# Optimization experiments

Measured on AMD Instinct MI355X. Metric: run time of the kernel, lower is better.

## Reference

```python
import jax, jax.numpy as jnp
import numpy as np

B, C, N, DI, DC = 64, 32, 1152, 8, 16
ROUTINGS = 3


def squash(x, axis=-1):
    sq = jnp.sum(x * x, axis=axis, keepdims=True)
    scale = sq / (1.0 + sq) / jnp.sqrt(sq + 1e-07)
    return scale * x


def setup_inputs() -> dict:
    key = jax.random.key(0)
    k1, k2 = jax.random.split(key)
    inputs = jax.random.normal(k1, (B, N, DI), dtype=jnp.float32)
    # Xavier-uniform init for W[n_caps, n_in, d_cap, d_in]; fan computed over last two dims
    limit = float(np.sqrt(6.0 / (DC + DI)))
    W = jax.random.uniform(k2, (C, N, DC, DI), dtype=jnp.float32, minval=-limit, maxval=limit)
    return {"inputs": inputs, "W": W}


def reference(inputs, W):
    # inputs_hat[b,c,n,i] = sum_j W[c,n,i,j] * inputs[b,n,j]
    inputs_hat = jnp.einsum('cnij,bnj->bcni', W, inputs)  # [B,C,N,DC]
    b = jnp.zeros((B, C, N), dtype=inputs_hat.dtype)
    outputs = None
    for i in range(ROUTINGS):
        c = jax.nn.softmax(b, axis=1)                      # over output capsules
        s = jnp.einsum('bcn,bcni->bci', c, inputs_hat)     # weighted sum over input caps
        outputs = squash(s)                                # [B,C,DC]
        if i < ROUTINGS - 1:
            agreement = jnp.einsum('bci,bcni->bcn', outputs, inputs_hat)
            b = b + agreement
    return outputs
```

## Files before the change

### kernel.cpp

```cpp
#include <hip/hip_runtime.h>
#include <hip/hip_bf16.h>
#include <hip/hip_fp16.h>

#define B_  64
#define C_  32
#define N_  1152
#define DI_ 8
#define DC_ 16
#define STH 512

#define HCH 2
#define HSLOT 192
#define NOCT 24

#define FCH 3
#define FSLOT 128

static __device__ __forceinline__ unsigned pkh(float a, float b) {
    __half2 t = __float22half2_rn(make_float2(a, b));
    return *reinterpret_cast<unsigned*>(&t);
}
static __device__ __forceinline__ float2 uph(unsigned u) {
    __half2 h; *reinterpret_cast<unsigned*>(&h) = u;
    return __half22float2(h);
}

__global__ __launch_bounds__(STH, 2) void caps_hat(
    const float* __restrict__ X, const float* __restrict__ W,
    uint4* __restrict__ hatg, __half2* __restrict__ p1)
{
    __shared__ float wlds[HCH * 64 * 64];

    const int xcd  = blockIdx.x & 7;
    const int k    = blockIdx.x >> 3;
    const int bg   = k & 3;
    const int slot = 24 * xcd + (k >> 2);

    const int tid  = threadIdx.x;
    const int lane = tid & 63;
    const int c    = lane & 31;
    const int h    = lane >> 5;
    const int le   = 2 * c + h;
    const int sw   = c & 7;
    const int wu   = __builtin_amdgcn_readfirstlane(tid) >> 6;
    const int bl0  = wu * 2;

    const int g_nl[4] = { (tid) >> 10, (tid + 512) >> 10, (tid + 1024) >> 10, (tid + 1536) >> 10 };
    const int g_f [4] = { (tid >> 4) & 63, ((tid + 512) >> 4) & 63, ((tid + 1024) >> 4) & 63, ((tid + 1536) >> 4) & 63 };
    const int g_q  = tid & 15;

    float acc[2][8];
#pragma unroll
    for (int bq = 0; bq < 2; bq++)
#pragma unroll
        for (int r = 0; r < 8; r++) acc[bq][r] = 0.f;

    float4 wreg[4];
    {
        const int n0 = slot * HCH;
#pragma unroll
        for (int i = 0; i < 4; i++) {
            const int wc = g_f[i] >> 1, wh = g_f[i] & 1;
            wreg[i] = *(const float4*)(W + (size_t)(wc * N_ + n0 + g_nl[i]) * 128 + wh * 64 + g_q * 4);
        }
#pragma unroll
        for (int i = 0; i < 4; i++) {
            const int wc = g_f[i] >> 1;
            *(float4*)(wlds + (g_nl[i] * 64 + g_f[i]) * 64 + (g_q ^ (wc & 7)) * 4) = wreg[i];
        }
    }
    __syncthreads();

    for (int cc = 0; cc < 3; cc++) {
        if (cc < 2) {
            const int n0 = (slot + (cc + 1) * HSLOT) * HCH;
#pragma unroll
            for (int i = 0; i < 4; i++) {
                const int wc = g_f[i] >> 1, wh = g_f[i] & 1;
                wreg[i] = *(const float4*)(W + (size_t)(wc * N_ + n0 + g_nl[i]) * 128 + wh * 64 + g_q * 4);
            }
        }
        const int n0 = (slot + cc * HSLOT) * HCH;

#pragma unroll
        for (int nl = 0; nl < HCH; nl++) {
            float4 xa[2], xb[2];
#pragma unroll
            for (int bq = 0; bq < 2; bq++) {
                const float* xp = X + ((size_t)(bg * 16 + bl0 + bq) * N_ + n0 + nl) * DI_;
                xa[bq] = *(const float4*)xp;
                xb[bq] = *(const float4*)(xp + 4);
            }
            uint4 hq[2];
            const float* frag = wlds + (nl * 64 + le) * 64;
#pragma unroll
            for (int rp = 0; rp < 4; rp++) {
                const int r0 = 2 * rp, r1 = r0 + 1;
                const int pa0 = ((2 * r0) ^ sw) * 4;
                const int pb0 = pa0 ^ 4;
                const int pa1 = ((2 * r1) ^ sw) * 4;
                const int pb1 = pa1 ^ 4;
                const float4 wa0 = *(const float4*)(frag + pa0);
                const float4 wb0 = *(const float4*)(frag + pb0);
                const float4 wa1 = *(const float4*)(frag + pa1);
                const float4 wb1 = *(const float4*)(frag + pb1);
#pragma unroll
                for (int bq = 0; bq < 2; bq++) {
                    const float hv0 = wa0.x*xa[bq].x + wa0.y*xa[bq].y + wa0.z*xa[bq].z + wa0.w*xa[bq].w
                                    + wb0.x*xb[bq].x + wb0.y*xb[bq].y + wb0.z*xb[bq].z + wb0.w*xb[bq].w;
                    const float hv1 = wa1.x*xa[bq].x + wa1.y*xa[bq].y + wa1.z*xa[bq].z + wa1.w*xa[bq].w
                                    + wb1.x*xb[bq].x + wb1.y*xb[bq].y + wb1.z*xb[bq].z + wb1.w*xb[bq].w;
                    acc[bq][r0] += hv0;
                    acc[bq][r1] += hv1;
                    (&hq[bq].x)[rp] = pkh(hv0, hv1);
                }
            }
#pragma unroll
            for (int bq = 0; bq < 2; bq++) {
                const int b = bg * 16 + bl0 + bq;
                hatg[(size_t)(b * N_ + n0 + nl) * 64 + le] = hq[bq];
            }
        }

        __syncthreads();
        if (cc < 2) {
#pragma unroll
            for (int i = 0; i < 4; i++) {
                const int wc = g_f[i] >> 1;
                *(float4*)(wlds + (g_nl[i] * 64 + g_f[i]) * 64 + (g_q ^ (wc & 7)) * 4) = wreg[i];
            }
            __syncthreads();
        }
    }

    __half2* pout = p1 + (size_t)(bg * HSLOT + slot) * (16 * 256);
#pragma unroll
    for (int bq = 0; bq < 2; bq++) {
        uint4 st;
        st.x = pkh(acc[bq][0]*0.03125f, acc[bq][1]*0.03125f);
        st.y = pkh(acc[bq][2]*0.03125f, acc[bq][3]*0.03125f);
        st.z = pkh(acc[bq][4]*0.03125f, acc[bq][5]*0.03125f);
        st.w = pkh(acc[bq][6]*0.03125f, acc[bq][7]*0.03125f);
        *(uint4*)(pout + (bl0 + bq) * 256 + le * 4) = st;
    }
}

__global__ __launch_bounds__(STH, 2) void caps_route(
    const uint4* __restrict__ hatg, const float* __restrict__ accb,
    float* __restrict__ p2)
{
    __shared__ float red[8 * 512];
    const int xcd  = blockIdx.x & 7;
    const int rest = blockIdx.x >> 3;
    const int ug   = rest % 3;
    const int b    = rest / 3;
    const int u    = 8 * ug + xcd;
    const int tid  = threadIdx.x;
    const int w    = tid >> 6;
    const int lane = tid & 63;
    const int c    = lane & 31;
    const int h    = lane >> 5;
    const int le   = 2 * c + h;

    const float* ap = accb + (size_t)b * 512 + le * 8;
    const float4 a0 = *(const float4*)ap;
    const float4 a1 = *(const float4*)(ap + 4);

    const uint4* hb = hatg + (size_t)(b * N_ + u * 48) * 64 + le;

    uint4 v[6];
#pragma unroll
    for (int m = 0; m < 6; m++)
        v[m] = hb[(size_t)(w + 8 * m) * 64];

    float lg[6], sm[6];
#pragma unroll
    for (int m = 0; m < 6; m++) {
        const float2 f0 = uph(v[m].x);
        const float2 f1 = uph(v[m].y);
        const float2 f2 = uph(v[m].z);
        const float2 f3 = uph(v[m].w);
        lg[m] = f0.x*a0.x + f0.y*a0.y + f1.x*a0.z + f1.y*a0.w
              + f2.x*a1.x + f2.y*a1.y + f3.x*a1.z + f3.y*a1.w;
    }
#pragma unroll
    for (int m = 0; m < 6; m++) lg[m] += __shfl_xor(lg[m], 32, 64);
#pragma unroll
    for (int m = 0; m < 6; m++) { lg[m] = __expf(lg[m]); sm[m] = lg[m]; }
#pragma unroll
    for (int d = 16; d >= 1; d >>= 1)
#pragma unroll
        for (int m = 0; m < 6; m++) sm[m] += __shfl_xor(sm[m], d, 64);

    float acc[8] = {0.f,0.f,0.f,0.f,0.f,0.f,0.f,0.f};
#pragma unroll
    for (int m = 0; m < 6; m++) {
        const float sc = lg[m] * __builtin_amdgcn_rcpf(sm[m]);
        const float2 f0 = uph(v[m].x);
        const float2 f1 = uph(v[m].y);
        const float2 f2 = uph(v[m].z);
        const float2 f3 = uph(v[m].w);
        acc[0] += sc * f0.x; acc[1] += sc * f0.y;
        acc[2] += sc * f1.x; acc[3] += sc * f1.y;
        acc[4] += sc * f2.x; acc[5] += sc * f2.y;
        acc[6] += sc * f3.x; acc[7] += sc * f3.y;
    }
    *(float4*)(red + w * 512 + le * 8)     = make_float4(acc[0], acc[1], acc[2], acc[3]);
    *(float4*)(red + w * 512 + le * 8 + 4) = make_float4(acc[4], acc[5], acc[6], acc[7]);
    __syncthreads();
    float vs = 0.f;
#pragma unroll
    for (int s = 0; s < 8; s++) vs += red[s * 512 + tid];
    p2[(size_t)(b * NOCT + u) * 512 + tid] = vs;
}

__global__ __launch_bounds__(512) void caps_r1(
    const __half2* __restrict__ p1, float* __restrict__ accb,
    float* __restrict__ out, int t)
{
    const int b   = blockIdx.x >> 2;
    const int q   = blockIdx.x & 3;
    const int tid = threadIdx.x;
    const int ep  = tid >> 3;
    const int p   = tid & 7;
    const int bg  = b >> 4, bl = b & 15;
    const __half2* base = p1 + (size_t)bg * HSLOT * 4096 + bl * 256 + (q * 64 + ep);
    float vx = 0.f, vy = 0.f;
#pragma unroll 8
    for (int ch = p; ch < HSLOT; ch += 8) {
        const float2 f = __half22float2(base[(size_t)ch * 4096]);
        vx += f.x; vy += f.y;
    }
    vx += __shfl_xor(vx, 1, 64);  vy += __shfl_xor(vy, 1, 64);
    vx += __shfl_xor(vx, 2, 64);  vy += __shfl_xor(vy, 2, 64);
    vx += __shfl_xor(vx, 4, 64);  vy += __shfl_xor(vy, 4, 64);
    float sq = vx * vx + vy * vy;
    sq += __shfl_xor(sq, 8, 64);
    sq += __shfl_xor(sq, 16, 64);
    sq += __shfl_xor(sq, 32, 64);
    const float scale = sq / (1.f + sq) * rsqrtf(sq + 1e-7f);
    if (p == 0) {
        const int oidx = b * 512 + q * 128 + ep * 2;
        const float ox = vx * scale, oy = vy * scale;
        if (t == 2) { out[oidx] = ox; out[oidx + 1] = oy; }
        else if (t == 0) { accb[oidx] = ox; accb[oidx + 1] = oy; }
        else { accb[oidx] += ox; accb[oidx + 1] += oy; }
    }
}

__global__ __launch_bounds__(512) void caps_r2(
    const float* __restrict__ p2, float* __restrict__ accb,
    float* __restrict__ out, int t)
{
    const int b = blockIdx.x;
    const int e = threadIdx.x;
    const float* base = p2 + (size_t)b * (NOCT * 512) + e;
    float v = 0.f;
#pragma unroll
    for (int s = 0; s < NOCT; s++) v += base[s * 512];
    float sq = v * v;
#pragma unroll
    for (int m = 1; m <= 8; m <<= 1) sq += __shfl_xor(sq, m, 64);
    const float scale = sq / (1.f + sq) * rsqrtf(sq + 1e-7f);
    const float ov = v * scale;
    const int oidx = b * 512 + e;
    if (t == 2) out[oidx] = ov;
    else        accb[oidx] += ov;
}

__global__ __launch_bounds__(STH, 2) void caps_s_fb(
    const float* __restrict__ X, const float* __restrict__ W,
    const float* __restrict__ aout, float* __restrict__ partials, int t)
{
    __shared__ float wlds[FCH * 64 * 64];
    __shared__ float xlds[FCH * 16 * 8];
    const int bg = blockIdx.x & 3, slot = blockIdx.x >> 2;
    const int tid = threadIdx.x, w = tid >> 6, lane = tid & 63;
    const int c = lane & 31, h = lane >> 5, bl0 = w * 2, sw = c & 7;
    float areg[2][8] = {};
    if (t > 0) {
#pragma unroll
        for (int bq = 0; bq < 2; bq++) {
            const float* ap = aout + (size_t)(bg * 16 + bl0 + bq) * 512 + c * 16 + h * 8;
            const float4 a0 = *(const float4*)ap; const float4 a1 = *(const float4*)(ap + 4);
            areg[bq][0]=a0.x; areg[bq][1]=a0.y; areg[bq][2]=a0.z; areg[bq][3]=a0.w;
            areg[bq][4]=a1.x; areg[bq][5]=a1.y; areg[bq][6]=a1.z; areg[bq][7]=a1.w;
        }
    }
    float acc[2][8];
#pragma unroll
    for (int bq = 0; bq < 2; bq++)
#pragma unroll
        for (int r = 0; r < 8; r++) acc[bq][r] = 0.f;
    for (int cc = 0; cc < 3; cc++) {
        if (cc) __syncthreads();
        const int n0 = (slot + cc * FSLOT) * FCH;
        for (int G = tid; G < FCH * 1024; G += STH) {
            const int nl = G >> 10, f = (G >> 4) & 63, q = G & 15;
            const int wc = f >> 1, wh = f & 1;
            const float4 v = *(const float4*)(W + (size_t)(wc * N_ + n0 + nl) * 128 + wh * 64 + q * 4);
            *(float4*)(wlds + (nl * 64 + f) * 64 + (q ^ (wc & 7)) * 4) = v;
        }
        if (tid < FCH * 32) {
            const int nl = tid >> 5, bl = (tid >> 1) & 15, qx = tid & 1;
            const float4 v = *(const float4*)(X + (size_t)((bg * 16 + bl) * N_ + n0 + nl) * DI_ + qx * 4);
            *(float4*)(xlds + (nl * 16 + bl) * 8 + qx * 4) = v;
        }
        __syncthreads();
#pragma unroll
        for (int nl = 0; nl < FCH; nl++) {
            float4 xa[2], xb[2];
#pragma unroll
            for (int bq = 0; bq < 2; bq++) {
                const float* xp = xlds + (nl * 16 + bl0 + bq) * 8;
                xa[bq] = *(const float4*)xp; xb[bq] = *(const float4*)(xp + 4);
            }
            float hat[2][8];
            const float* frag = wlds + (nl * 64 + 2 * c + h) * 64;
#pragma unroll
            for (int r = 0; r < 8; r++) {
                const int pa = ((2 * r) ^ sw) * 4; const int pb = pa ^ 4;
                const float4 wa = *(const float4*)(frag + pa);
                const float4 wb = *(const float4*)(frag + pb);
#pragma unroll
                for (int bq = 0; bq < 2; bq++)
                    hat[bq][r] = wa.x*xa[bq].x + wa.y*xa[bq].y + wa.z*xa[bq].z + wa.w*xa[bq].w
                               + wb.x*xb[bq].x + wb.y*xb[bq].y + wb.z*xb[bq].z + wb.w*xb[bq].w;
            }
#pragma unroll
            for (int bq = 0; bq < 2; bq++) {
                float softc;
                if (t > 0) {
                    float lg = hat[bq][0]*areg[bq][0] + hat[bq][1]*areg[bq][1]
                             + hat[bq][2]*areg[bq][2] + hat[bq][3]*areg[bq][3]
                             + hat[bq][4]*areg[bq][4] + hat[bq][5]*areg[bq][5]
                             + hat[bq][6]*areg[bq][6] + hat[bq][7]*areg[bq][7];
                    lg += __shfl_xor(lg, 32, 64);
                    const float e = __expf(lg);
                    float s = e;
#pragma unroll
                    for (int m = 16; m >= 1; m >>= 1) s += __shfl_xor(s, m, 64);
                    softc = e / s;
                } else softc = 1.0f / 32.0f;
#pragma unroll
                for (int r = 0; r < 8; r++) acc[bq][r] += softc * hat[bq][r];
            }
        }
    }
    float* pout = partials + (size_t)(bg * FSLOT + slot) * (16 * 512);
#pragma unroll
    for (int bq = 0; bq < 2; bq++) {
        float* pb = pout + (bl0 + bq) * 512 + c * 16 + h * 8;
        *(float4*)pb       = make_float4(acc[bq][0], acc[bq][1], acc[bq][2], acc[bq][3]);
        *(float4*)(pb + 4) = make_float4(acc[bq][4], acc[bq][5], acc[bq][6], acc[bq][7]);
    }
}

__global__ __launch_bounds__(256) void caps_r1_fb(
    const float* __restrict__ partials, float* __restrict__ accb,
    float* __restrict__ out, int t)
{
    const int b   = blockIdx.x >> 2;
    const int q   = blockIdx.x & 3;
    const int tid = threadIdx.x;
    const int e   = q * 128 + (tid >> 1);
    const int p   = tid & 1;
    const int bg  = b >> 4, bl = b & 15;
    const float* base = partials + (size_t)bg * FSLOT * 8192 + (size_t)bl * 512 + e;
    float v = 0.f;
#pragma unroll 8
    for (int ch = p; ch < FSLOT; ch += 2)
        v += base[(size_t)ch * 8192];
    v += __shfl_xor(v, 1, 64);
    float sq = v * v;
#pragma unroll
    for (int m = 2; m <= 16; m <<= 1) sq += __shfl_xor(sq, m, 64);
    const float scale = sq / (1.f + sq) * rsqrtf(sq + 1e-7f);
    const float ov = v * scale;
    if (p == 0) {
        const int oidx = b * 512 + e;
        if (t == 2) out[oidx] = ov;
        else        accb[oidx] = (t == 0) ? ov : (accb[oidx] + ov);
    }
}

extern "C" void kernel_launch(void* const* d_in, const int* in_sizes, int n_in,
                              void* d_out, int out_size, void* d_ws, size_t ws_size,
                              hipStream_t stream) {
    const float* X = (const float*)d_in[0];
    const float* W = (const float*)d_in[1];
    float* out = (float*)d_out;

    const size_t hat_b = (size_t)B_ * N_ * 512 * 2;
    const size_t p1_b  = (size_t)4 * HSLOT * 4096 * 4;
    const size_t p2_b  = (size_t)B_ * NOCT * 512 * 4;
    const size_t acc_b = (size_t)B_ * 512 * 4;

    if (ws_size >= hat_b + p1_b + p2_b + acc_b) {
        char* ws = (char*)d_ws;
        uint4*   hatg = (uint4*)ws;
        __half2* p1   = (__half2*)(ws + hat_b);
        float*   p2   = (float*)(ws + hat_b + p1_b);
        float*   accb = (float*)(ws + hat_b + p1_b + p2_b);
        caps_hat  <<<768, STH, 0, stream>>>(X, W, hatg, p1);
        caps_r1   <<<256, 512, 0, stream>>>(p1, accb, out, 0);
        caps_route<<<B_ * NOCT, STH, 0, stream>>>(hatg, accb, p2);
        caps_r2   <<<64, 512, 0, stream>>>(p2, accb, out, 1);
        caps_route<<<B_ * NOCT, STH, 0, stream>>>(hatg, accb, p2);
        caps_r2   <<<64, 512, 0, stream>>>(p2, accb, out, 2);
    } else {
        float* partials = (float*)d_ws;
        float* accb = partials + (size_t)512 * 8192;
        for (int t = 0; t < 3; t++) {
            caps_s_fb<<<512, STH, 0, stream>>>(X, W, accb, partials, t);
            caps_r1_fb<<<256, 256, 0, stream>>>(partials, accb, out, t);
        }
    }
}
```

Baseline: 144.1 us.

## Halve batch per block in caps_hat, drop W register prefetch, split route softmax

caps_hat now gives each block 8 batch rows instead of 16, with one batch per wave, and launches twice as many blocks. The W register double-buffer is replaced by a plain load-to-LDS then sync each chunk. This cuts register pressure and raises parallelism, but every W tile is loaded from global memory twice as often and the W load is no longer overlapped with compute. caps_route's softmax is split into two groups of three to shorten live ranges, and the p1 layout and caps_r1 indexing are adjusted to match.

After: 129.7 us. -10.0%, faster.

```diff
diff --git a/kernel.cpp b/kernel.cpp
--- a/kernel.cpp
+++ b/kernel.cpp
@@ -33,8 +33,8 @@
 
     const int xcd  = blockIdx.x & 7;
     const int k    = blockIdx.x >> 3;
-    const int bg   = k & 3;
-    const int slot = 24 * xcd + (k >> 2);
+    const int bg   = k & 7;
+    const int slot = 24 * xcd + (k >> 3);
 
     const int tid  = threadIdx.x;
     const int lane = tid & 63;
@@ -43,55 +43,31 @@
     const int le   = 2 * c + h;
     const int sw   = c & 7;
     const int wu   = __builtin_amdgcn_readfirstlane(tid) >> 6;
-    const int bl0  = wu * 2;
-
-    const int g_nl[4] = { (tid) >> 10, (tid + 512) >> 10, (tid + 1024) >> 10, (tid + 1536) >> 10 };
-    const int g_f [4] = { (tid >> 4) & 63, ((tid + 512) >> 4) & 63, ((tid + 1024) >> 4) & 63, ((tid + 1536) >> 4) & 63 };
-    const int g_q  = tid & 15;
-
-    float acc[2][8];
-#pragma unroll
-    for (int bq = 0; bq < 2; bq++)
-#pragma unroll
-        for (int r = 0; r < 8; r++) acc[bq][r] = 0.f;
-
-    float4 wreg[4];
-    {
-        const int n0 = slot * HCH;
-#pragma unroll
-        for (int i = 0; i < 4; i++) {
-            const int wc = g_f[i] >> 1, wh = g_f[i] & 1;
-            wreg[i] = *(const float4*)(W + (size_t)(wc * N_ + n0 + g_nl[i]) * 128 + wh * 64 + g_q * 4);
-        }
-#pragma unroll
-        for (int i = 0; i < 4; i++) {
-            const int wc = g_f[i] >> 1;
-            *(float4*)(wlds + (g_nl[i] * 64 + g_f[i]) * 64 + (g_q ^ (wc & 7)) * 4) = wreg[i];
-        }
-    }
-    __syncthreads();
+    const int b    = bg * 8 + wu;
+
+    float acc[8];
+#pragma unroll
+    for (int r = 0; r < 8; r++) acc[r] = 0.f;
 
     for (int cc = 0; cc < 3; cc++) {
-        if (cc < 2) {
-            const int n0 = (slot + (cc + 1) * HSLOT) * HCH;
-#pragma unroll
-            for (int i = 0; i < 4; i++) {
-                const int wc = g_f[i] >> 1, wh = g_f[i] & 1;
-                wreg[i] = *(const float4*)(W + (size_t)(wc * N_ + n0 + g_nl[i]) * 128 + wh * 64 + g_q * 4);
-            }
-        }
+        if (cc) __syncthreads();
         const int n0 = (slot + cc * HSLOT) * HCH;
 
 #pragma unroll
+        for (int G = tid; G < HCH * 1024; G += STH) {
+            const int nl = G >> 10, f = (G >> 4) & 63, q = G & 15;
+            const int wc = f >> 1, wh = f & 1;
+            const float4 v = *(const float4*)(W + (size_t)(wc * N_ + n0 + nl) * 128 + wh * 64 + q * 4);
+            *(float4*)(wlds + (nl * 64 + f) * 64 + (q ^ (wc & 7)) * 4) = v;
+        }
+        __syncthreads();
+
+#pragma unroll
         for (int nl = 0; nl < HCH; nl++) {
-            float4 xa[2], xb[2];
-#pragma unroll
-            for (int bq = 0; bq < 2; bq++) {
-                const float* xp = X + ((size_t)(bg * 16 + bl0 + bq) * N_ + n0 + nl) * DI_;
-                xa[bq] = *(const float4*)xp;
-                xb[bq] = *(const float4*)(xp + 4);
-            }
-            uint4 hq[2];
+            const float* xp = X + ((size_t)b * N_ + n0 + nl) * DI_;
+            const float4 xa = *(const float4*)xp;
+            const float4 xb = *(const float4*)(xp + 4);
+            uint4 hq;
             const float* frag = wlds + (nl * 64 + le) * 64;
 #pragma unroll
             for (int rp = 0; rp < 4; rp++) {
@@ -104,45 +80,25 @@
                 const float4 wb0 = *(const float4*)(frag + pb0);
                 const float4 wa1 = *(const float4*)(frag + pa1);
                 const float4 wb1 = *(const float4*)(frag + pb1);
-#pragma unroll
-                for (int bq = 0; bq < 2; bq++) {
-                    const float hv0 = wa0.x*xa[bq].x + wa0.y*xa[bq].y + wa0.z*xa[bq].z + wa0.w*xa[bq].w
-                                    + wb0.x*xb[bq].x + wb0.y*xb[bq].y + wb0.z*xb[bq].z + wb0.w*xb[bq].w;
-                    const float hv1 = wa1.x*xa[bq].x + wa1.y*xa[bq].y + wa1.z*xa[bq].z + wa1.w*xa[bq].w
-                                    + wb1.x*xb[bq].x + wb1.y*xb[bq].y + wb1.z*xb[bq].z + wb1.w*xb[bq].w;
-                    acc[bq][r0] += hv0;
-                    acc[bq][r1] += hv1;
-                    (&hq[bq].x)[rp] = pkh(hv0, hv1);
-                }
+                const float hv0 = wa0.x*xa.x + wa0.y*xa.y + wa0.z*xa.z + wa0.w*xa.w
+                                + wb0.x*xb.x + wb0.y*xb.y + wb0.z*xb.z + wb0.w*xb.w;
+                const float hv1 = wa1.x*xa.x + wa1.y*xa.y + wa1.z*xa.z + wa1.w*xa.w
+                                + wb1.x*xb.x + wb1.y*xb.y + wb1.z*xb.z + wb1.w*xb.w;
+                acc[r0] += hv0;
+                acc[r1] += hv1;
+                (&hq.x)[rp] = pkh(hv0, hv1);
             }
-#pragma unroll
-            for (int bq = 0; bq < 2; bq++) {
-                const int b = bg * 16 + bl0 + bq;
-                hatg[(size_t)(b * N_ + n0 + nl) * 64 + le] = hq[bq];
-            }
-        }
-
-        __syncthreads();
-        if (cc < 2) {
-#pragma unroll
-            for (int i = 0; i < 4; i++) {
-                const int wc = g_f[i] >> 1;
-                *(float4*)(wlds + (g_nl[i] * 64 + g_f[i]) * 64 + (g_q ^ (wc & 7)) * 4) = wreg[i];
-            }
-            __syncthreads();
-        }
-    }
-
-    __half2* pout = p1 + (size_t)(bg * HSLOT + slot) * (16 * 256);
-#pragma unroll
-    for (int bq = 0; bq < 2; bq++) {
-        uint4 st;
-        st.x = pkh(acc[bq][0]*0.03125f, acc[bq][1]*0.03125f);
-        st.y = pkh(acc[bq][2]*0.03125f, acc[bq][3]*0.03125f);
-        st.z = pkh(acc[bq][4]*0.03125f, acc[bq][5]*0.03125f);
-        st.w = pkh(acc[bq][6]*0.03125f, acc[bq][7]*0.03125f);
-        *(uint4*)(pout + (bl0 + bq) * 256 + le * 4) = st;
-    }
+            hatg[(size_t)(b * N_ + n0 + nl) * 64 + le] = hq;
+        }
+    }
+
+    __half2* pout = p1 + (size_t)(bg * HSLOT + slot) * (8 * 256);
+    uint4 st;
+    st.x = pkh(acc[0]*0.03125f, acc[1]*0.03125f);
+    st.y = pkh(acc[2]*0.03125f, acc[3]*0.03125f);
+    st.z = pkh(acc[4]*0.03125f, acc[5]*0.03125f);
+    st.w = pkh(acc[6]*0.03125f, acc[7]*0.03125f);
+    *(uint4*)(pout + wu * 256 + le * 4) = st;
 }
 
 __global__ __launch_bounds__(STH, 2) void caps_route(
@@ -173,37 +129,41 @@
     for (int m = 0; m < 6; m++)
         v[m] = hb[(size_t)(w + 8 * m) * 64];
 
-    float lg[6], sm[6];
-#pragma unroll
-    for (int m = 0; m < 6; m++) {
-        const float2 f0 = uph(v[m].x);
-        const float2 f1 = uph(v[m].y);
-        const float2 f2 = uph(v[m].z);
-        const float2 f3 = uph(v[m].w);
-        lg[m] = f0.x*a0.x + f0.y*a0.y + f1.x*a0.z + f1.y*a0.w
-              + f2.x*a1.x + f2.y*a1.y + f3.x*a1.z + f3.y*a1.w;
-    }
-#pragma unroll
-    for (int m = 0; m < 6; m++) lg[m] += __shfl_xor(lg[m], 32, 64);
-#pragma unroll
-    for (int m = 0; m < 6; m++) { lg[m] = __expf(lg[m]); sm[m] = lg[m]; }
-#pragma unroll
-    for (int d = 16; d >= 1; d >>= 1)
-#pragma unroll
-        for (int m = 0; m < 6; m++) sm[m] += __shfl_xor(sm[m], d, 64);
-
     float acc[8] = {0.f,0.f,0.f,0.f,0.f,0.f,0.f,0.f};
 #pragma unroll
-    for (int m = 0; m < 6; m++) {
-        const float sc = lg[m] * __builtin_amdgcn_rcpf(sm[m]);
-        const float2 f0 = uph(v[m].x);
-        const float2 f1 = uph(v[m].y);
-        const float2 f2 = uph(v[m].z);
-        const float2 f3 = uph(v[m].w);
-        acc[0] += sc * f0.x; acc[1] += sc * f0.y;
-        acc[2] += sc * f1.x; acc[3] += sc * f1.y;
-        acc[4] += sc * f2.x; acc[5] += sc * f2.y;
-        acc[6] += sc * f3.x; acc[7] += sc * f3.y;
+    for (int g = 0; g < 2; g++) {
+        float lg[3], sm[3];
+#pragma unroll
+        for (int j = 0; j < 3; j++) {
+            const uint4 vv = v[g * 3 + j];
+            const float2 f0 = uph(vv.x);
+            const float2 f1 = uph(vv.y);
+            const float2 f2 = uph(vv.z);
+            const float2 f3 = uph(vv.w);
+            lg[j] = f0.x*a0.x + f0.y*a0.y + f1.x*a0.z + f1.y*a0.w
+                  + f2.x*a1.x + f2.y*a1.y + f3.x*a1.z + f3.y*a1.w;
+        }
+#pragma unroll
+        for (int j = 0; j < 3; j++) lg[j] += __shfl_xor(lg[j], 32, 64);
+#pragma unroll
+        for (int j = 0; j < 3; j++) { lg[j] = __expf(lg[j]); sm[j] = lg[j]; }
+#pragma unroll
+        for (int d = 16; d >= 1; d >>= 1)
+#pragma unroll
+            for (int j = 0; j < 3; j++) sm[j] += __shfl_xor(sm[j], d, 64);
+#pragma unroll
+        for (int j = 0; j < 3; j++) {
+            const float sc = lg[j] * __builtin_amdgcn_rcpf(sm[j]);
+            const uint4 vv = v[g * 3 + j];
+            const float2 f0 = uph(vv.x);
+            const float2 f1 = uph(vv.y);
+            const float2 f2 = uph(vv.z);
+            const float2 f3 = uph(vv.w);
+            acc[0] += sc * f0.x; acc[1] += sc * f0.y;
+            acc[2] += sc * f1.x; acc[3] += sc * f1.y;
+            acc[4] += sc * f2.x; acc[5] += sc * f2.y;
+            acc[6] += sc * f3.x; acc[7] += sc * f3.y;
+        }
     }
     *(float4*)(red + w * 512 + le * 8)     = make_float4(acc[0], acc[1], acc[2], acc[3]);
     *(float4*)(red + w * 512 + le * 8 + 4) = make_float4(acc[4], acc[5], acc[6], acc[7]);
@@ -223,12 +183,12 @@
     const int tid = threadIdx.x;
     const int ep  = tid >> 3;
     const int p   = tid & 7;
-    const int bg  = b >> 4, bl = b & 15;
-    const __half2* base = p1 + (size_t)bg * HSLOT * 4096 + bl * 256 + (q * 64 + ep);
+    const int bg  = b >> 3, bl = b & 7;
+    const __half2* base = p1 + (size_t)bg * HSLOT * 2048 + bl * 256 + (q * 64 + ep);
     float vx = 0.f, vy = 0.f;
 #pragma unroll 8
     for (int ch = p; ch < HSLOT; ch += 8) {
-        const float2 f = __half22float2(base[(size_t)ch * 4096]);
+        const float2 f = __half22float2(base[(size_t)ch * 2048]);
         vx += f.x; vy += f.y;
     }
     vx += __shfl_xor(vx, 1, 64);  vy += __shfl_xor(vy, 1, 64);
@@ -392,7 +352,7 @@
     float* out = (float*)d_out;
 
     const size_t hat_b = (size_t)B_ * N_ * 512 * 2;
-    const size_t p1_b  = (size_t)4 * HSLOT * 4096 * 4;
+    const size_t p1_b  = (size_t)8 * HSLOT * 2048 * 4;
     const size_t p2_b  = (size_t)B_ * NOCT * 512 * 4;
     const size_t acc_b = (size_t)B_ * 512 * 4;
 
@@ -402,7 +362,7 @@
         __half2* p1   = (__half2*)(ws + hat_b);
         float*   p2   = (float*)(ws + hat_b + p1_b);
         float*   accb = (float*)(ws + hat_b + p1_b + p2_b);
-        caps_hat  <<<768, STH, 0, stream>>>(X, W, hatg, p1);
+        caps_hat  <<<1536, STH, 0, stream>>>(X, W, hatg, p1);
         caps_r1   <<<256, 512, 0, stream>>>(p1, accb, out, 0);
         caps_route<<<B_ * NOCT, STH, 0, stream>>>(hatg, accb, p2);
         caps_r2   <<<64, 512, 0, stream>>>(p2, accb, out, 1);
```
